# Kernel tuning notes

Measured on AMD Instinct MI355X. Metric: run time of the kernel, lower is better.

Reference implementation:

```python
import jax, jax.numpy as jnp
import numpy as np
import math

N_HEADS = 12
HEAD_DIM = 64
D_MODEL = 768
BATCH = 2
SEQ = 2048
GRID = 46  # num_patches_per_side


def _rope_1d(x, pos, dim):
    # x: (B,S,H,dim), pos: (S,) int -> rotary embedding along last dim
    inv_freq = 1.0 / (10000.0 ** (jnp.arange(0, dim, 2, dtype=jnp.float32) / dim))  # (dim/2,)
    ang = pos.astype(jnp.float32)[:, None] * inv_freq  # (S, dim/2)
    cos = jnp.concatenate([jnp.cos(ang), jnp.cos(ang)], axis=-1)[None, :, None, :]
    sin = jnp.concatenate([jnp.sin(ang), jnp.sin(ang)], axis=-1)[None, :, None, :]
    x1, x2 = jnp.split(x, 2, axis=-1)
    rot = jnp.concatenate([-x2, x1], axis=-1)
    return x * cos.astype(x.dtype) + rot * sin.astype(x.dtype)


def _rope_2d(x, row_ids, col_ids):
    # 2D RoPE: first half of head_dim rotated by row position, second half by column position
    half = x.shape[-1] // 2
    xr = _rope_1d(x[..., :half], row_ids, half)
    xc = _rope_1d(x[..., half:], col_ids, half)
    return jnp.concatenate([xr, xc], axis=-1)


def setup_inputs() -> dict:
    key = jax.random.key(0)
    ks = jax.random.split(key, 7)
    scale = 1.0 / math.sqrt(D_MODEL)
    return {
        "x": jax.random.normal(ks[0], (BATCH, SEQ, D_MODEL), dtype=jnp.float32),
        "row_ids": jax.random.randint(ks[1], (SEQ,), 0, GRID),
        "col_ids": jax.random.randint(ks[2], (SEQ,), 0, GRID),
        "Wq": jax.random.normal(ks[3], (D_MODEL, D_MODEL), dtype=jnp.float32) * scale,
        "Wk": jax.random.normal(ks[4], (D_MODEL, D_MODEL), dtype=jnp.float32) * scale,
        "Wv": jax.random.normal(ks[5], (D_MODEL, D_MODEL), dtype=jnp.float32) * scale,
        "Wo": jax.random.normal(ks[6], (D_MODEL, D_MODEL), dtype=jnp.float32) * scale,
    }


def reference(x, row_ids, col_ids, Wq, Wk, Wv, Wo):
    B, S, _ = x.shape
    # projections (nn.Linear: y = x @ W.T)
    q = (x @ Wq.T).reshape(B, S, N_HEADS, HEAD_DIM)
    k = (x @ Wk.T).reshape(B, S, N_HEADS, HEAD_DIM)
    v = (x @ Wv.T).reshape(B, S, N_HEADS, HEAD_DIM)
    q = _rope_2d(q, row_ids, col_ids)
    k = _rope_2d(k, row_ids, col_ids)
    # (B,H,S,D)
    q = q.transpose(0, 2, 1, 3)
    k = k.transpose(0, 2, 1, 3)
    v = v.transpose(0, 2, 1, 3)
    scale = 1.0 / math.sqrt(HEAD_DIM)
    scores = jnp.einsum('bhqd,bhkd->bhqk', q, k) * scale  # (B,H,S,S)
    causal = jnp.triu(jnp.ones((S, S), dtype=bool), k=1)
    scores = jnp.where(causal, -jnp.inf, scores)
    attn = jax.nn.softmax(scores, axis=-1)
    out = jnp.einsum('bhqk,bhkd->bhqd', attn, v)
    out = out.transpose(0, 2, 1, 3).reshape(B, S, D_MODEL)
    return out @ Wo.T
```

## Files before the change

### kernel.cpp

```cpp
#include <hip/hip_runtime.h>
#include <stdint.h>
#include <stddef.h>

#define DEV __device__ __forceinline__

typedef unsigned short u16;
typedef __attribute__((ext_vector_type(8))) __bf16 bf16x8;
typedef __attribute__((ext_vector_type(4))) float f32x4;
typedef __attribute__((ext_vector_type(8))) unsigned short u16x8;
typedef __attribute__((ext_vector_type(4))) unsigned short u16x4;

DEV u16 f2bf(float f) {
  uint32_t u = __builtin_bit_cast(uint32_t, f);
  u += 0x7fffu + ((u >> 16) & 1u);
  return (u16)(u >> 16);
}
DEV float bf2f(u16 h) {
  uint32_t u = ((uint32_t)h) << 16;
  return __builtin_bit_cast(float, u);
}
DEV f32x4 mfma16(bf16x8 a, bf16x8 b, f32x4 c) {
  return __builtin_amdgcn_mfma_f32_16x16x32_bf16(a, b, c, 0, 0, 0);
}
DEV void ld_lds16(const void* g, void* l) {
  __builtin_amdgcn_global_load_lds((const __attribute__((address_space(1))) void*)g,
                                   (__attribute__((address_space(3))) void*)l, 16, 0, 0);
}

#define Q_SCALE 0.18033688011112042f

__global__ __launch_bounds__(256) void k_cvt_all(const float* __restrict__ x,
                                                 const float* __restrict__ wq,
                                                 const float* __restrict__ wk,
                                                 const float* __restrict__ wv,
                                                 const float* __restrict__ wo,
                                                 u16* __restrict__ dx,
                                                 u16* __restrict__ dqkv,
                                                 u16* __restrict__ dwo) {
  const int bid = blockIdx.x;
  const float* src;
  u16* dst;
  int off;
  if (bid < 3072) {
    src = x; dst = dx; off = bid;
  } else {
    const int t = bid - 3072;
    const int w = t / 576;
    off = t - w * 576;
    src = (w == 0) ? wq : (w == 1) ? wk : (w == 2) ? wv : wo;
    dst = (w < 3) ? (dqkv + (size_t)w * 589824) : dwo;
  }
  const int i = (off * 256 + threadIdx.x) * 4;
  const float4 f = *(const float4*)(src + i);
  u16x4 o;
  o.x = f2bf(f.x); o.y = f2bf(f.y); o.z = f2bf(f.z); o.w = f2bf(f.w);
  *(u16x4*)(dst + i) = o;
}

__global__ __launch_bounds__(256) void k_gemm_qkv(const u16* __restrict__ A,
                                                  const u16* __restrict__ B,
                                                  const int* __restrict__ row_ids,
                                                  const int* __restrict__ col_ids,
                                                  u16* __restrict__ Qh,
                                                  u16* __restrict__ Kh,
                                                  u16* __restrict__ Vt) {
  const int K = 768;
  __shared__ __align__(16) u16 sA[128 * 64];
  __shared__ __align__(16) u16 sB[128 * 64];
  __shared__ int sIds[256];
  const int tid = threadIdx.x;
  const int lane = tid & 63;
  const int wid = tid >> 6;
  const int wm = wid & 1, wn = wid >> 1;
  const int col16 = lane & 15, quad = lane >> 4;
  const int rowBase = blockIdx.y * 128;
  const int colBase = blockIdx.x * 128;
  const int seg_r = lane >> 3;
  const int seg_c = lane & 7;

  f32x4 zero; zero[0] = zero[1] = zero[2] = zero[3] = 0.0f;
  f32x4 acc[4][4];
#pragma unroll
  for (int i = 0; i < 4; ++i)
#pragma unroll
    for (int j = 0; j < 4; ++j) acc[i][j] = zero;

  for (int k0 = 0; k0 < K; k0 += 64) {
#pragma unroll
    for (int c = 0; c < 4; ++c) {
      const int seg = wid * 4 + c;
      ld_lds16(A + (size_t)(rowBase + seg * 8 + seg_r) * K + k0 + seg_c * 8, sA + seg * 512);
      ld_lds16(B + (size_t)(colBase + seg * 8 + seg_r) * K + k0 + seg_c * 8, sB + seg * 512);
    }
    __syncthreads();
#pragma unroll
    for (int kk = 0; kk < 2; ++kk) {
      bf16x8 af[4], bfr[4];
#pragma unroll
      for (int t = 0; t < 4; ++t) {
        af[t]  = *(const bf16x8*)(sA + (wm * 64 + t * 16 + col16) * 64 + kk * 32 + quad * 8);
        bfr[t] = *(const bf16x8*)(sB + (wn * 64 + t * 16 + col16) * 64 + kk * 32 + quad * 8);
      }
#pragma unroll
      for (int tm = 0; tm < 4; ++tm)
#pragma unroll
        for (int tn = 0; tn < 4; ++tn)
          acc[tm][tn] = mfma16(af[tm], bfr[tn], acc[tm][tn]);
    }
    __syncthreads();
  }

  const int bx = blockIdx.x;
  const int type = bx / 6;
  const int h = (bx % 6) * 2 + wn;
  const int bb = rowBase >> 11;
  const int s0 = rowBase & 2047;
  const size_t bh = (size_t)bb * 12 + h;

  if (type < 2) {
    if (tid < 128) {
      sIds[tid] = row_ids[s0 + tid];
      sIds[128 + tid] = col_ids[s0 + tid];
    }
    __syncthreads();
    u16* dst = (type == 0) ? Qh : Kh;
    const float scl = (type == 0) ? Q_SCALE : 1.0f;
    const float invf = exp2f(-(float)col16 * 0.8304820237218406f);
#pragma unroll
    for (int tm = 0; tm < 4; ++tm)
#pragma unroll
      for (int r = 0; r < 4; ++r) {
        const int lrow = wm * 64 + tm * 16 + quad * 4 + r;
        const float aR = (float)sIds[lrow] * invf;
        const float aC = (float)sIds[128 + lrow] * invf;
        const float cR = __cosf(aR), sR = __sinf(aR);
        const float cC = __cosf(aC), sC = __sinf(aC);
        const float x1 = acc[tm][0][r], x2 = acc[tm][1][r];
        const float x3 = acc[tm][2][r], x4 = acc[tm][3][r];
        u16* p = dst + (bh * 2048 + s0 + lrow) * 64;
        p[col16]      = f2bf((x1 * cR - x2 * sR) * scl);
        p[col16 + 16] = f2bf((x2 * cR + x1 * sR) * scl);
        p[col16 + 32] = f2bf((x3 * cC - x4 * sC) * scl);
        p[col16 + 48] = f2bf((x4 * cC + x3 * sC) * scl);
      }
  } else {
#pragma unroll
    for (int tm = 0; tm < 4; ++tm)
#pragma unroll
      for (int tn = 0; tn < 4; ++tn) {
        const int d = tn * 16 + col16;
        const int srow = s0 + wm * 64 + tm * 16 + quad * 4;
        u16x4 o4;
#pragma unroll
        for (int r = 0; r < 4; ++r) o4[r] = f2bf(acc[tm][tn][r]);
        *(u16x4*)(Vt + (bh * 64 + d) * 2048 + srow) = o4;
      }
  }
}

__global__ __launch_bounds__(256, 3) void k_gemm_o(const u16* __restrict__ A,
                                                   const u16* __restrict__ B,
                                                   float* __restrict__ C,
                                                   int N, int K) {
  __shared__ __align__(16) u16 sA[64 * 72];
  __shared__ __align__(16) u16 sB[64 * 72];
  const int tid = threadIdx.x;
  const int lane = tid & 63;
  const int wid = tid >> 6;
  const int col16 = lane & 15, quad = lane >> 4;
  const int wm = wid & 1, wn = wid >> 1;
  const int rowBase = blockIdx.y * 64;
  const int colBase = blockIdx.x * 64;
  const int sr = tid >> 3;
  const int sc8 = (tid & 7) * 8;

  f32x4 zero; zero[0] = zero[1] = zero[2] = zero[3] = 0.0f;
  f32x4 acc[2][2];
  acc[0][0] = zero; acc[0][1] = zero; acc[1][0] = zero; acc[1][1] = zero;

  u16x8 ar[2], br[2];
  auto gload = [&](int k0) {
    ar[0] = *(const u16x8*)(A + (size_t)(rowBase + sr) * K + k0 + sc8);
    ar[1] = *(const u16x8*)(A + (size_t)(rowBase + 32 + sr) * K + k0 + sc8);
    br[0] = *(const u16x8*)(B + (size_t)(colBase + sr) * K + k0 + sc8);
    br[1] = *(const u16x8*)(B + (size_t)(colBase + 32 + sr) * K + k0 + sc8);
  };

  gload(0);
  for (int k0 = 0; k0 < K; k0 += 64) {
    __syncthreads();
    *(u16x8*)&sA[sr * 72 + sc8] = ar[0];
    *(u16x8*)&sA[(32 + sr) * 72 + sc8] = ar[1];
    *(u16x8*)&sB[sr * 72 + sc8] = br[0];
    *(u16x8*)&sB[(32 + sr) * 72 + sc8] = br[1];
    if (k0 + 64 < K) gload(k0 + 64);
    __syncthreads();
#pragma unroll
    for (int kk = 0; kk < 2; ++kk) {
      bf16x8 af[2], bfr[2];
#pragma unroll
      for (int t = 0; t < 2; ++t) {
        af[t]  = *(const bf16x8*)&sA[(wm * 32 + t * 16 + col16) * 72 + kk * 32 + quad * 8];
        bfr[t] = *(const bf16x8*)&sB[(wn * 32 + t * 16 + col16) * 72 + kk * 32 + quad * 8];
      }
#pragma unroll
      for (int tm = 0; tm < 2; ++tm)
#pragma unroll
        for (int tn = 0; tn < 2; ++tn)
          acc[tm][tn] = mfma16(af[tm], bfr[tn], acc[tm][tn]);
    }
  }

#pragma unroll
  for (int tm = 0; tm < 2; ++tm)
#pragma unroll
    for (int tn = 0; tn < 2; ++tn)
#pragma unroll
      for (int r = 0; r < 4; ++r) {
        const int row = rowBase + wm * 32 + tm * 16 + quad * 4 + r;
        const int col = colBase + wn * 32 + tn * 16 + col16;
        C[(size_t)row * N + col] = acc[tm][tn][r];
      }
}

__global__ __launch_bounds__(256, 3) void k_attn(const u16* __restrict__ Qh,
                                                 const u16* __restrict__ Kh,
                                                 const u16* __restrict__ Vt,
                                                 u16* __restrict__ O,
                                                 u16* __restrict__ Opart,
                                                 float* __restrict__ ml) {
  __shared__ __align__(16) u16 sK[2][64 * 72];
  __shared__ __align__(16) u16 sV[2][64 * 72];
  __shared__ __align__(16) u16 sP[4][16 * 72];
  const int tid = threadIdx.x;
  const int lane = tid & 63;
  const int wid = tid >> 6;
  const int col16 = lane & 15;
  const int quad = lane >> 4;
  const int bx = blockIdx.x;
  const int bh = bx / 80;
  const int u = bx - bh * 80;
  int qt, c;
  if (u < 8)       { qt = u; c = 0; }
  else if (u < 24) { const int t = u - 8;  qt = 8 + (t >> 1); c = t & 1; }
  else if (u < 48) { const int t = u - 24; const int q3 = t / 3; qt = 16 + q3; c = t - q3 * 3; }
  else             { const int t = u - 48; qt = 24 + (t >> 2); c = t & 3; }
  const int nc = (qt >> 3) + 1;
  const int tile0 = c * 8;
  const int tileE = min(tile0 + 8, qt + 1);
  const int ntiles = tileE - tile0;
  const int b = bh / 12, h = bh % 12;
  const int qw = qt * 64 + wid * 16;

  const u16* Qb = Qh + (size_t)bh * (2048 * 64);
  const u16* Kb = Kh + (size_t)bh * (2048 * 64);
  const u16* Vb = Vt + (size_t)bh * (64 * 2048);

  const bf16x8 bQ0 = *(const bf16x8*)(Qb + (size_t)(qw + col16) * 64 + quad * 8);
  const bf16x8 bQ1 = *(const bf16x8*)(Qb + (size_t)(qw + col16) * 64 + 32 + quad * 8);

  f32x4 zero; zero[0] = zero[1] = zero[2] = zero[3] = 0.0f;
  f32x4 o[4];
#pragma unroll
  for (int i = 0; i < 4; ++i) o[i] = zero;
  float m_r = -1e30f, l_r = 0.0f;

  u16* sPw = &sP[wid][0];

  const int sr = tid >> 3;
  const int sc8 = (tid & 7) * 8;
  u16x8 kr[2], vr[2];
  auto gload = [&](int kt) {
#pragma unroll
    for (int i = 0; i < 2; ++i) {
      kr[i] = *(const u16x8*)(Kb + (size_t)(kt + sr + i * 32) * 64 + sc8);
      vr[i] = *(const u16x8*)(Vb + (size_t)(sr + i * 32) * 2048 + kt + sc8);
    }
  };
  auto lwrite = [&](int buf) {
#pragma unroll
    for (int i = 0; i < 2; ++i) {
      *(u16x8*)&sK[buf][(sr + i * 32) * 72 + sc8] = kr[i];
      *(u16x8*)&sV[buf][(sr + i * 32) * 72 + sc8] = vr[i];
    }
  };

  gload(tile0 * 64);
  lwrite(0);
  if (ntiles > 1) gload((tile0 + 1) * 64);
  __syncthreads();

  for (int ki = 0; ki < ntiles; ++ki) {
    const int buf = ki & 1;
    const int kt = (tile0 + ki) * 64;
    if (ki + 1 < ntiles) {
      lwrite(buf ^ 1);
      if (ki + 2 < ntiles) gload((tile0 + ki + 2) * 64);
    }
    bf16x8 ka0[4], ka1[4];
#pragma unroll
    for (int tn = 0; tn < 4; ++tn) {
      const int base = (tn * 16 + col16) * 72 + quad * 8;
      ka0[tn] = *(const bf16x8*)&sK[buf][base];
      ka1[tn] = *(const bf16x8*)&sK[buf][base + 32];
    }
    f32x4 sc[4];
#pragma unroll
    for (int tn = 0; tn < 4; ++tn)
      sc[tn] = mfma16(ka1[tn], bQ1, mfma16(ka0[tn], bQ0, zero));
    bf16x8 va0[4], va1[4];
#pragma unroll
    for (int tn = 0; tn < 4; ++tn) {
      const int base = (tn * 16 + col16) * 72 + quad * 8;
      va0[tn] = *(const bf16x8*)&sV[buf][base];
      va1[tn] = *(const bf16x8*)&sV[buf][base + 32];
    }
    if (kt + 63 > qw) {
#pragma unroll
      for (int tn = 0; tn < 4; ++tn)
#pragma unroll
        for (int rr = 0; rr < 4; ++rr)
          if (kt + tn * 16 + quad * 4 + rr > qw + col16) sc[tn][rr] = -1e30f;
    }
    float vm = sc[0][0];
#pragma unroll
    for (int tn = 0; tn < 4; ++tn)
#pragma unroll
      for (int rr = 0; rr < 4; ++rr) vm = fmaxf(vm, sc[tn][rr]);
    vm = fmaxf(vm, __shfl_xor(vm, 16, 64));
    vm = fmaxf(vm, __shfl_xor(vm, 32, 64));
    const float mn = fmaxf(m_r, vm);
    const float alpha = exp2f(m_r - mn);
    m_r = mn;
    float rs = 0.0f;
#pragma unroll
    for (int tn = 0; tn < 4; ++tn)
#pragma unroll
      for (int h2 = 0; h2 < 2; ++h2) {
        const float p0 = exp2f(sc[tn][2 * h2] - mn);
        const float p1 = exp2f(sc[tn][2 * h2 + 1] - mn);
        const uint32_t u0 = __builtin_bit_cast(uint32_t, p0) & 0xffff0000u;
        const uint32_t u1 = __builtin_bit_cast(uint32_t, p1) & 0xffff0000u;
        rs += __builtin_bit_cast(float, u0) + __builtin_bit_cast(float, u1);
        ((uint32_t*)sPw)[col16 * 36 + tn * 8 + quad * 2 + h2] = u1 | (u0 >> 16);
      }
    rs += __shfl_xor(rs, 16, 64);
    rs += __shfl_xor(rs, 32, 64);
    l_r = l_r * alpha + rs;
#pragma unroll
    for (int t = 0; t < 4; ++t)
#pragma unroll
      for (int rr = 0; rr < 4; ++rr) o[t][rr] *= alpha;
    asm volatile("s_waitcnt lgkmcnt(0)" ::: "memory");
    const bf16x8 bP0 = *(const bf16x8*)(sPw + col16 * 72 + quad * 8);
    const bf16x8 bP1 = *(const bf16x8*)(sPw + col16 * 72 + 32 + quad * 8);
#pragma unroll
    for (int tn = 0; tn < 4; ++tn)
      o[tn] = mfma16(va1[tn], bP1, mfma16(va0[tn], bP0, o[tn]));
    __syncthreads();
  }

  if (nc == 1) {
    const float invl = 1.0f / l_r;
    const size_t row = (size_t)b * 2048 + qw + col16;
#pragma unroll
    for (int tn = 0; tn < 4; ++tn)
#pragma unroll
      for (int h2 = 0; h2 < 2; ++h2) {
        const float v0 = o[tn][2 * h2] * invl;
        const float v1 = o[tn][2 * h2 + 1] * invl;
        const uint32_t w = (uint32_t)f2bf(v0) | ((uint32_t)f2bf(v1) << 16);
        const int col = h * 64 + tn * 16 + quad * 4 + 2 * h2;
        *(uint32_t*)(O + row * 768 + col) = w;
      }
  } else {
    u16* op = Opart + (size_t)bx * 4096 + (wid * 16 + col16) * 64;
#pragma unroll
    for (int tn = 0; tn < 4; ++tn)
#pragma unroll
      for (int h2 = 0; h2 < 2; ++h2) {
        const uint32_t w = (uint32_t)f2bf(o[tn][2 * h2]) | ((uint32_t)f2bf(o[tn][2 * h2 + 1]) << 16);
        *(uint32_t*)(op + tn * 16 + quad * 4 + 2 * h2) = w;
      }
    if (quad == 0) {
      float* mlp = ml + (size_t)bx * 128;
      mlp[wid * 16 + col16] = m_r;
      mlp[64 + wid * 16 + col16] = l_r;
    }
  }
}

__global__ __launch_bounds__(256) void k_combine(const u16* __restrict__ Opart,
                                                 const float* __restrict__ ml,
                                                 u16* __restrict__ O) {
  const int bx = blockIdx.x;
  const int bh = bx / 24;
  const int qt = 8 + (bx - bh * 24);
  const int b = bh / 12, h = bh % 12;
  const int nc = (qt >> 3) + 1;
  const int prefix = (qt < 16) ? (8 + 2 * (qt - 8))
                   : (qt < 24) ? (24 + 3 * (qt - 16))
                               : (48 + 4 * (qt - 24));
  const int slot0 = bh * 80 + prefix;
  const int tid = threadIdx.x;
  const int r = tid >> 2;
  const int d0 = (tid & 3) * 16;

  float m_i[4], w_i[4];
  float M = -1e30f;
  for (int i = 0; i < nc; ++i) {
    m_i[i] = ml[(size_t)(slot0 + i) * 128 + r];
    M = fmaxf(M, m_i[i]);
  }
  float l = 0.0f;
  for (int i = 0; i < nc; ++i) {
    w_i[i] = exp2f(m_i[i] - M);
    l += w_i[i] * ml[(size_t)(slot0 + i) * 128 + 64 + r];
  }
  const float invl = 1.0f / l;

  float a[16];
#pragma unroll
  for (int j = 0; j < 16; ++j) a[j] = 0.0f;
  for (int i = 0; i < nc; ++i) {
    const u16* op = Opart + (size_t)(slot0 + i) * 4096 + r * 64 + d0;
    const u16x8 v0 = *(const u16x8*)op;
    const u16x8 v1 = *(const u16x8*)(op + 8);
#pragma unroll
    for (int j = 0; j < 8; ++j) {
      a[j] += w_i[i] * bf2f(v0[j]);
      a[8 + j] += w_i[i] * bf2f(v1[j]);
    }
  }
  u16x8 o0, o1;
#pragma unroll
  for (int j = 0; j < 8; ++j) {
    o0[j] = f2bf(a[j] * invl);
    o1[j] = f2bf(a[8 + j] * invl);
  }
  u16* dst = O + (size_t)(b * 2048 + qt * 64 + r) * 768 + h * 64 + d0;
  *(u16x8*)dst = o0;
  *(u16x8*)(dst + 8) = o1;
}

extern "C" void kernel_launch(void* const* d_in, const int* in_sizes, int n_in,
                              void* d_out, int out_size, void* d_ws, size_t ws_size,
                              hipStream_t stream) {
  const float* x       = (const float*)d_in[0];
  const int*   row_ids = (const int*)d_in[1];
  const int*   col_ids = (const int*)d_in[2];
  const float* Wq      = (const float*)d_in[3];
  const float* Wk      = (const float*)d_in[4];
  const float* Wv      = (const float*)d_in[5];
  const float* Wo      = (const float*)d_in[6];
  float* out = (float*)d_out;

  uint8_t* w8 = (uint8_t*)d_ws;
  u16* x_bf = (u16*)(w8 + 0);
  u16* wqkv = (u16*)(w8 + 6291456);
  u16* wo   = (u16*)(w8 + 9830400);
  u16* qh   = (u16*)(w8 + 29884416);
  u16* kh   = (u16*)(w8 + 36175872);
  u16* vt   = (u16*)(w8 + 42467328);
  u16* obuf = (u16*)(w8 + 48758784);
  u16*   opart = (u16*)(w8 + 11010048);
  float* mlbuf = (float*)(w8 + 11010048 + 15728640);

  k_cvt_all<<<5376, 256, 0, stream>>>(x, Wq, Wk, Wv, Wo, x_bf, wqkv, wo);
  k_gemm_qkv<<<dim3(18, 32), 256, 0, stream>>>(x_bf, wqkv, row_ids, col_ids, qh, kh, vt);
  k_attn<<<1920, 256, 0, stream>>>(qh, kh, vt, obuf, opart, mlbuf);
  k_combine<<<576, 256, 0, stream>>>(opart, mlbuf, obuf);
  k_gemm_o<<<dim3(12, 64), 256, 0, stream>>>(obuf, wo, out, 768, 768);
}
```

Before: 184.0 us.

## Process two query tiles per attention block to reuse K/V loads

Each attention block now handles 128 query rows (two 64-row groups per wave) instead of 64, so every K/V tile staged in LDS feeds twice as many MFMAs and the block count is halved. Block ordering is remapped to interleave heads and put the longest work first. The online-softmax rescale is skipped when the running max does not grow. The combine kernel and partial-buffer layout are updated to match, at the cost of more registers per thread and fewer blocks to fill the GPU.

```diff
diff --git a/kernel.cpp b/kernel.cpp
--- a/kernel.cpp
+++ b/kernel.cpp
@@ -238,32 +238,42 @@
   const int col16 = lane & 15;
   const int quad = lane >> 4;
   const int bx = blockIdx.x;
-  const int bh = bx / 80;
-  const int u = bx - bh * 80;
-  int qt, c;
-  if (u < 8)       { qt = u; c = 0; }
-  else if (u < 24) { const int t = u - 8;  qt = 8 + (t >> 1); c = t & 1; }
-  else if (u < 48) { const int t = u - 24; const int q3 = t / 3; qt = 16 + q3; c = t - q3 * 3; }
-  else             { const int t = u - 48; qt = 24 + (t >> 2); c = t & 3; }
-  const int nc = (qt >> 3) + 1;
+  const int b3 = bx & 7;
+  const int r_ = bx >> 3;
+  const int g_ = r_ / 40;
+  const int u = 39 - (r_ - g_ * 40);
+  const int bh = b3 + 8 * g_;
+  int qt2, c;
+  if (u < 4)       { qt2 = u; c = 0; }
+  else if (u < 12) { const int t = u - 4;  qt2 = 4 + (t >> 1); c = t & 1; }
+  else if (u < 24) { const int t = u - 12; const int q3 = t / 3; qt2 = 8 + q3; c = t - q3 * 3; }
+  else             { const int t = u - 24; qt2 = 12 + (t >> 2); c = t & 3; }
+  const int nc = (qt2 >> 2) + 1;
+  const int totTiles = 2 * qt2 + 2;
   const int tile0 = c * 8;
-  const int tileE = min(tile0 + 8, qt + 1);
-  const int ntiles = tileE - tile0;
+  const int ntiles = min(8, totTiles - tile0);
   const int b = bh / 12, h = bh % 12;
-  const int qw = qt * 64 + wid * 16;
+  const int qs0 = qt2 * 128 + wid * 16;
 
   const u16* Qb = Qh + (size_t)bh * (2048 * 64);
   const u16* Kb = Kh + (size_t)bh * (2048 * 64);
   const u16* Vb = Vt + (size_t)bh * (64 * 2048);
 
-  const bf16x8 bQ0 = *(const bf16x8*)(Qb + (size_t)(qw + col16) * 64 + quad * 8);
-  const bf16x8 bQ1 = *(const bf16x8*)(Qb + (size_t)(qw + col16) * 64 + 32 + quad * 8);
+  bf16x8 bQ[2][2];
+#pragma unroll
+  for (int g = 0; g < 2; ++g) {
+    const u16* qp = Qb + (size_t)(qs0 + g * 64 + col16) * 64 + quad * 8;
+    bQ[g][0] = *(const bf16x8*)qp;
+    bQ[g][1] = *(const bf16x8*)(qp + 32);
+  }
 
   f32x4 zero; zero[0] = zero[1] = zero[2] = zero[3] = 0.0f;
-  f32x4 o[4];
-#pragma unroll
-  for (int i = 0; i < 4; ++i) o[i] = zero;
-  float m_r = -1e30f, l_r = 0.0f;
+  f32x4 o[2][4];
+#pragma unroll
+  for (int g = 0; g < 2; ++g)
+#pragma unroll
+    for (int i = 0; i < 4; ++i) o[g][i] = zero;
+  float m_r[2] = {-1e30f, -1e30f}, l_r[2] = {0.0f, 0.0f};
 
   u16* sPw = &sP[wid][0];
 
@@ -304,10 +314,12 @@
       ka0[tn] = *(const bf16x8*)&sK[buf][base];
       ka1[tn] = *(const bf16x8*)&sK[buf][base + 32];
     }
-    f32x4 sc[4];
-#pragma unroll
-    for (int tn = 0; tn < 4; ++tn)
-      sc[tn] = mfma16(ka1[tn], bQ1, mfma16(ka0[tn], bQ0, zero));
+    f32x4 sc[2][4];
+#pragma unroll
+    for (int tn = 0; tn < 4; ++tn) {
+      sc[0][tn] = mfma16(ka1[tn], bQ[0][1], mfma16(ka0[tn], bQ[0][0], zero));
+      sc[1][tn] = mfma16(ka1[tn], bQ[1][1], mfma16(ka0[tn], bQ[1][0], zero));
+    }
     bf16x8 va0[4], va1[4];
 #pragma unroll
     for (int tn = 0; tn < 4; ++tn) {
@@ -315,77 +327,93 @@
       va0[tn] = *(const bf16x8*)&sV[buf][base];
       va1[tn] = *(const bf16x8*)&sV[buf][base + 32];
     }
-    if (kt + 63 > qw) {
+#pragma unroll
+    for (int g = 0; g < 2; ++g) {
+      const int qw = qs0 + g * 64;
+      if (kt + 63 > qw) {
+#pragma unroll
+        for (int tn = 0; tn < 4; ++tn)
+#pragma unroll
+          for (int rr = 0; rr < 4; ++rr)
+            if (kt + tn * 16 + quad * 4 + rr > qw + col16) sc[g][tn][rr] = -1e30f;
+      }
+      float vm = sc[g][0][0];
 #pragma unroll
       for (int tn = 0; tn < 4; ++tn)
 #pragma unroll
-        for (int rr = 0; rr < 4; ++rr)
-          if (kt + tn * 16 + quad * 4 + rr > qw + col16) sc[tn][rr] = -1e30f;
-    }
-    float vm = sc[0][0];
-#pragma unroll
-    for (int tn = 0; tn < 4; ++tn)
-#pragma unroll
-      for (int rr = 0; rr < 4; ++rr) vm = fmaxf(vm, sc[tn][rr]);
-    vm = fmaxf(vm, __shfl_xor(vm, 16, 64));
-    vm = fmaxf(vm, __shfl_xor(vm, 32, 64));
-    const float mn = fmaxf(m_r, vm);
-    const float alpha = exp2f(m_r - mn);
-    m_r = mn;
-    float rs = 0.0f;
-#pragma unroll
-    for (int tn = 0; tn < 4; ++tn)
-#pragma unroll
-      for (int h2 = 0; h2 < 2; ++h2) {
-        const float p0 = exp2f(sc[tn][2 * h2] - mn);
-        const float p1 = exp2f(sc[tn][2 * h2 + 1] - mn);
-        const uint32_t u0 = __builtin_bit_cast(uint32_t, p0) & 0xffff0000u;
-        const uint32_t u1 = __builtin_bit_cast(uint32_t, p1) & 0xffff0000u;
-        rs += __builtin_bit_cast(float, u0) + __builtin_bit_cast(float, u1);
-        ((uint32_t*)sPw)[col16 * 36 + tn * 8 + quad * 2 + h2] = u1 | (u0 >> 16);
-      }
-    rs += __shfl_xor(rs, 16, 64);
-    rs += __shfl_xor(rs, 32, 64);
-    l_r = l_r * alpha + rs;
-#pragma unroll
-    for (int t = 0; t < 4; ++t)
-#pragma unroll
-      for (int rr = 0; rr < 4; ++rr) o[t][rr] *= alpha;
-    asm volatile("s_waitcnt lgkmcnt(0)" ::: "memory");
-    const bf16x8 bP0 = *(const bf16x8*)(sPw + col16 * 72 + quad * 8);
-    const bf16x8 bP1 = *(const bf16x8*)(sPw + col16 * 72 + 32 + quad * 8);
-#pragma unroll
-    for (int tn = 0; tn < 4; ++tn)
-      o[tn] = mfma16(va1[tn], bP1, mfma16(va0[tn], bP0, o[tn]));
+        for (int rr = 0; rr < 4; ++rr) vm = fmaxf(vm, sc[g][tn][rr]);
+      vm = fmaxf(vm, __shfl_xor(vm, 16, 64));
+      vm = fmaxf(vm, __shfl_xor(vm, 32, 64));
+      if (__any(vm > m_r[g])) {
+        const float mn = fmaxf(m_r[g], vm);
+        const float alpha = exp2f(m_r[g] - mn);
+        m_r[g] = mn;
+        l_r[g] *= alpha;
+#pragma unroll
+        for (int t = 0; t < 4; ++t)
+#pragma unroll
+          for (int rr = 0; rr < 4; ++rr) o[g][t][rr] *= alpha;
+      }
+      const float mn = m_r[g];
+      float rs = 0.0f;
+#pragma unroll
+      for (int tn = 0; tn < 4; ++tn)
+#pragma unroll
+        for (int h2 = 0; h2 < 2; ++h2) {
+          const float p0 = exp2f(sc[g][tn][2 * h2] - mn);
+          const float p1 = exp2f(sc[g][tn][2 * h2 + 1] - mn);
+          const uint32_t u0 = __builtin_bit_cast(uint32_t, p0) & 0xffff0000u;
+          const uint32_t u1 = __builtin_bit_cast(uint32_t, p1) & 0xffff0000u;
+          rs += __builtin_bit_cast(float, u0) + __builtin_bit_cast(float, u1);
+          ((uint32_t*)sPw)[col16 * 36 + tn * 8 + quad * 2 + h2] = u1 | (u0 >> 16);
+        }
+      rs += __shfl_xor(rs, 16, 64);
+      rs += __shfl_xor(rs, 32, 64);
+      l_r[g] += rs;
+      asm volatile("s_waitcnt lgkmcnt(0)" ::: "memory");
+      const bf16x8 bP0 = *(const bf16x8*)(sPw + col16 * 72 + quad * 8);
+      const bf16x8 bP1 = *(const bf16x8*)(sPw + col16 * 72 + 32 + quad * 8);
+#pragma unroll
+      for (int tn = 0; tn < 4; ++tn)
+        o[g][tn] = mfma16(va1[tn], bP1, mfma16(va0[tn], bP0, o[g][tn]));
+    }
     __syncthreads();
   }
 
   if (nc == 1) {
-    const float invl = 1.0f / l_r;
-    const size_t row = (size_t)b * 2048 + qw + col16;
-#pragma unroll
-    for (int tn = 0; tn < 4; ++tn)
-#pragma unroll
-      for (int h2 = 0; h2 < 2; ++h2) {
-        const float v0 = o[tn][2 * h2] * invl;
-        const float v1 = o[tn][2 * h2 + 1] * invl;
-        const uint32_t w = (uint32_t)f2bf(v0) | ((uint32_t)f2bf(v1) << 16);
-        const int col = h * 64 + tn * 16 + quad * 4 + 2 * h2;
-        *(uint32_t*)(O + row * 768 + col) = w;
-      }
+#pragma unroll
+    for (int g = 0; g < 2; ++g) {
+      const float invl = 1.0f / l_r[g];
+      const size_t row = (size_t)b * 2048 + qs0 + g * 64 + col16;
+#pragma unroll
+      for (int tn = 0; tn < 4; ++tn)
+#pragma unroll
+        for (int h2 = 0; h2 < 2; ++h2) {
+          const float v0 = o[g][tn][2 * h2] * invl;
+          const float v1 = o[g][tn][2 * h2 + 1] * invl;
+          const uint32_t w = (uint32_t)f2bf(v0) | ((uint32_t)f2bf(v1) << 16);
+          const int col = h * 64 + tn * 16 + quad * 4 + 2 * h2;
+          *(uint32_t*)(O + row * 768 + col) = w;
+        }
+    }
   } else {
-    u16* op = Opart + (size_t)bx * 4096 + (wid * 16 + col16) * 64;
-#pragma unroll
-    for (int tn = 0; tn < 4; ++tn)
-#pragma unroll
-      for (int h2 = 0; h2 < 2; ++h2) {
-        const uint32_t w = (uint32_t)f2bf(o[tn][2 * h2]) | ((uint32_t)f2bf(o[tn][2 * h2 + 1]) << 16);
-        *(uint32_t*)(op + tn * 16 + quad * 4 + 2 * h2) = w;
-      }
-    if (quad == 0) {
-      float* mlp = ml + (size_t)bx * 128;
-      mlp[wid * 16 + col16] = m_r;
-      mlp[64 + wid * 16 + col16] = l_r;
+#pragma unroll
+    for (int g = 0; g < 2; ++g) {
+      const int prow = g * 64 + wid * 16 + col16;
+      u16* op = Opart + (size_t)bx * 8192 + prow * 64;
+#pragma unroll
+      for (int tn = 0; tn < 4; ++tn)
+#pragma unroll
+        for (int h2 = 0; h2 < 2; ++h2) {
+          const uint32_t w = (uint32_t)f2bf(o[g][tn][2 * h2]) |
+                             ((uint32_t)f2bf(o[g][tn][2 * h2 + 1]) << 16);
+          *(uint32_t*)(op + tn * 16 + quad * 4 + 2 * h2) = w;
+        }
+      if (quad == 0) {
+        float* mlp = ml + (size_t)bx * 256;
+        mlp[prow] = m_r[g];
+        mlp[128 + prow] = l_r[g];
+      }
     }
   }
 }
@@ -394,53 +422,55 @@
                                                  const float* __restrict__ ml,
                                                  u16* __restrict__ O) {
   const int bx = blockIdx.x;
-  const int bh = bx / 24;
-  const int qt = 8 + (bx - bh * 24);
+  const int bh = bx / 12;
+  const int qt2 = 4 + (bx - bh * 12);
   const int b = bh / 12, h = bh % 12;
-  const int nc = (qt >> 3) + 1;
-  const int prefix = (qt < 16) ? (8 + 2 * (qt - 8))
-                   : (qt < 24) ? (24 + 3 * (qt - 16))
-                               : (48 + 4 * (qt - 24));
-  const int slot0 = bh * 80 + prefix;
+  const int nc = (qt2 >> 2) + 1;
+  const int uBase = (qt2 < 8) ? (4 + 2 * (qt2 - 4))
+                  : (qt2 < 12) ? (12 + 3 * (qt2 - 8))
+                               : (24 + 4 * (qt2 - 12));
+  const int hb3 = bh & 7, hg = bh >> 3;
   const int tid = threadIdx.x;
-  const int r = tid >> 2;
-  const int d0 = (tid & 3) * 16;
+  const int r = tid >> 1;
+  const int d0 = (tid & 1) * 32;
+
+  int slots[4];
+  for (int i = 0; i < nc; ++i)
+    slots[i] = ((hg * 40 + 39 - (uBase + i)) << 3) | hb3;
 
   float m_i[4], w_i[4];
   float M = -1e30f;
   for (int i = 0; i < nc; ++i) {
-    m_i[i] = ml[(size_t)(slot0 + i) * 128 + r];
+    m_i[i] = ml[(size_t)slots[i] * 256 + r];
     M = fmaxf(M, m_i[i]);
   }
   float l = 0.0f;
   for (int i = 0; i < nc; ++i) {
     w_i[i] = exp2f(m_i[i] - M);
-    l += w_i[i] * ml[(size_t)(slot0 + i) * 128 + 64 + r];
+    l += w_i[i] * ml[(size_t)slots[i] * 256 + 128 + r];
   }
   const float invl = 1.0f / l;
 
-  float a[16];
-#pragma unroll
-  for (int j = 0; j < 16; ++j) a[j] = 0.0f;
+  float a[32];
+#pragma unroll
+  for (int j = 0; j < 32; ++j) a[j] = 0.0f;
   for (int i = 0; i < nc; ++i) {
-    const u16* op = Opart + (size_t)(slot0 + i) * 4096 + r * 64 + d0;
-    const u16x8 v0 = *(const u16x8*)op;
-    const u16x8 v1 = *(const u16x8*)(op + 8);
-#pragma unroll
-    for (int j = 0; j < 8; ++j) {
-      a[j] += w_i[i] * bf2f(v0[j]);
-      a[8 + j] += w_i[i] * bf2f(v1[j]);
-    }
-  }
-  u16x8 o0, o1;
-#pragma unroll
-  for (int j = 0; j < 8; ++j) {
-    o0[j] = f2bf(a[j] * invl);
-    o1[j] = f2bf(a[8 + j] * invl);
-  }
-  u16* dst = O + (size_t)(b * 2048 + qt * 64 + r) * 768 + h * 64 + d0;
-  *(u16x8*)dst = o0;
-  *(u16x8*)(dst + 8) = o1;
+    const u16* op = Opart + (size_t)slots[i] * 8192 + r * 64 + d0;
+#pragma unroll
+    for (int v = 0; v < 4; ++v) {
+      const u16x8 vv = *(const u16x8*)(op + v * 8);
+#pragma unroll
+      for (int j = 0; j < 8; ++j) a[v * 8 + j] += w_i[i] * bf2f(vv[j]);
+    }
+  }
+  u16* dst = O + (size_t)(b * 2048 + qt2 * 128 + r) * 768 + h * 64 + d0;
+#pragma unroll
+  for (int v = 0; v < 4; ++v) {
+    u16x8 ov;
+#pragma unroll
+    for (int j = 0; j < 8; ++j) ov[j] = f2bf(a[v * 8 + j] * invl);
+    *(u16x8*)(dst + v * 8) = ov;
+  }
 }
 
 extern "C" void kernel_launch(void* const* d_in, const int* in_sizes, int n_in,
@@ -468,7 +498,7 @@
 
   k_cvt_all<<<5376, 256, 0, stream>>>(x, Wq, Wk, Wv, Wo, x_bf, wqkv, wo);
   k_gemm_qkv<<<dim3(18, 32), 256, 0, stream>>>(x_bf, wqkv, row_ids, col_ids, qh, kh, vt);
-  k_attn<<<1920, 256, 0, stream>>>(qh, kh, vt, obuf, opart, mlbuf);
-  k_combine<<<576, 256, 0, stream>>>(opart, mlbuf, obuf);
+  k_attn<<<960, 256, 0, stream>>>(qh, kh, vt, obuf, opart, mlbuf);
+  k_combine<<<288, 256, 0, stream>>>(opart, mlbuf, obuf);
   k_gemm_o<<<dim3(12, 64), 256, 0, stream>>>(obuf, wo, out, 768, 768);
 }
```

Result: no change. 187.4 us (+1.9%).

## Shrink QKV GEMM tile to 64 rows, pack RoPE stores, widen conversion loads

Applied to the files above, without the earlier changes.

The QKV projection GEMM now uses 64x128 tiles, so twice as many blocks launch and each wave owns one 32-column RoPE half. That lets each lane compute a single sin/cos pair and write packed 32-bit pairs. The output dims within each half are permuted identically for Q and K, so the dot products are unchanged. The fp32-to-bf16 conversion kernel handles 8 elements per thread with 16-byte stores, and the attention P conversion now rounds to nearest instead of truncating. The smaller tile reloads B from memory more often, in exchange for better occupancy and lighter epilogue work.

```diff
diff --git a/kernel.cpp b/kernel.cpp
--- a/kernel.cpp
+++ b/kernel.cpp
@@ -41,70 +41,74 @@
   const float* src;
   u16* dst;
   int off;
-  if (bid < 3072) {
+  if (bid < 1536) {
     src = x; dst = dx; off = bid;
   } else {
-    const int t = bid - 3072;
-    const int w = t / 576;
-    off = t - w * 576;
+    const int t = bid - 1536;
+    const int w = t / 288;
+    off = t - w * 288;
     src = (w == 0) ? wq : (w == 1) ? wk : (w == 2) ? wv : wo;
     dst = (w < 3) ? (dqkv + (size_t)w * 589824) : dwo;
   }
-  const int i = (off * 256 + threadIdx.x) * 4;
-  const float4 f = *(const float4*)(src + i);
-  u16x4 o;
-  o.x = f2bf(f.x); o.y = f2bf(f.y); o.z = f2bf(f.z); o.w = f2bf(f.w);
-  *(u16x4*)(dst + i) = o;
-}
-
-__global__ __launch_bounds__(256) void k_gemm_qkv(const u16* __restrict__ A,
-                                                  const u16* __restrict__ B,
-                                                  const int* __restrict__ row_ids,
-                                                  const int* __restrict__ col_ids,
-                                                  u16* __restrict__ Qh,
-                                                  u16* __restrict__ Kh,
-                                                  u16* __restrict__ Vt) {
+  const int i = (off * 256 + threadIdx.x) * 8;
+  const float4 f0 = *(const float4*)(src + i);
+  const float4 f1 = *(const float4*)(src + i + 4);
+  u16x8 o;
+  o[0] = f2bf(f0.x); o[1] = f2bf(f0.y); o[2] = f2bf(f0.z); o[3] = f2bf(f0.w);
+  o[4] = f2bf(f1.x); o[5] = f2bf(f1.y); o[6] = f2bf(f1.z); o[7] = f2bf(f1.w);
+  *(u16x8*)(dst + i) = o;
+}
+
+__global__ __launch_bounds__(256, 4) void k_gemm_qkv(const u16* __restrict__ A,
+                                                     const u16* __restrict__ B,
+                                                     const int* __restrict__ row_ids,
+                                                     const int* __restrict__ col_ids,
+                                                     u16* __restrict__ Qh,
+                                                     u16* __restrict__ Kh,
+                                                     u16* __restrict__ Vt) {
   const int K = 768;
-  __shared__ __align__(16) u16 sA[128 * 64];
+  __shared__ __align__(16) u16 sA[64 * 64];
   __shared__ __align__(16) u16 sB[128 * 64];
-  __shared__ int sIds[256];
+  __shared__ int sIds[128];
   const int tid = threadIdx.x;
   const int lane = tid & 63;
   const int wid = tid >> 6;
-  const int wm = wid & 1, wn = wid >> 1;
   const int col16 = lane & 15, quad = lane >> 4;
-  const int rowBase = blockIdx.y * 128;
+  const int rowBase = blockIdx.y * 64;
   const int colBase = blockIdx.x * 128;
   const int seg_r = lane >> 3;
   const int seg_c = lane & 7;
 
   f32x4 zero; zero[0] = zero[1] = zero[2] = zero[3] = 0.0f;
-  f32x4 acc[4][4];
-#pragma unroll
-  for (int i = 0; i < 4; ++i)
-#pragma unroll
-    for (int j = 0; j < 4; ++j) acc[i][j] = zero;
+  f32x4 acc[4][2];
+#pragma unroll
+  for (int i = 0; i < 4; ++i) { acc[i][0] = zero; acc[i][1] = zero; }
 
   for (int k0 = 0; k0 < K; k0 += 64) {
+#pragma unroll
+    for (int c = 0; c < 2; ++c) {
+      const int seg = wid * 2 + c;
+      ld_lds16(A + (size_t)(rowBase + seg * 8 + seg_r) * K + k0 + seg_c * 8, sA + seg * 512);
+    }
 #pragma unroll
     for (int c = 0; c < 4; ++c) {
       const int seg = wid * 4 + c;
-      ld_lds16(A + (size_t)(rowBase + seg * 8 + seg_r) * K + k0 + seg_c * 8, sA + seg * 512);
       ld_lds16(B + (size_t)(colBase + seg * 8 + seg_r) * K + k0 + seg_c * 8, sB + seg * 512);
     }
     __syncthreads();
 #pragma unroll
     for (int kk = 0; kk < 2; ++kk) {
-      bf16x8 af[4], bfr[4];
-#pragma unroll
-      for (int t = 0; t < 4; ++t) {
-        af[t]  = *(const bf16x8*)(sA + (wm * 64 + t * 16 + col16) * 64 + kk * 32 + quad * 8);
-        bfr[t] = *(const bf16x8*)(sB + (wn * 64 + t * 16 + col16) * 64 + kk * 32 + quad * 8);
-      }
+      bf16x8 af[4], bfr[2];
+#pragma unroll
+      for (int t = 0; t < 4; ++t)
+        af[t] = *(const bf16x8*)(sA + (t * 16 + col16) * 64 + kk * 32 + quad * 8);
+#pragma unroll
+      for (int t = 0; t < 2; ++t)
+        bfr[t] = *(const bf16x8*)(sB + (wid * 32 + t * 16 + col16) * 64 + kk * 32 + quad * 8);
 #pragma unroll
       for (int tm = 0; tm < 4; ++tm)
 #pragma unroll
-        for (int tn = 0; tn < 4; ++tn)
+        for (int tn = 0; tn < 2; ++tn)
           acc[tm][tn] = mfma16(af[tm], bfr[tn], acc[tm][tn]);
     }
     __syncthreads();
@@ -112,44 +116,41 @@
 
   const int bx = blockIdx.x;
   const int type = bx / 6;
-  const int h = (bx % 6) * 2 + wn;
+  const int h = (bx % 6) * 2 + (wid >> 1);
+  const int half = wid & 1;
   const int bb = rowBase >> 11;
   const int s0 = rowBase & 2047;
   const size_t bh = (size_t)bb * 12 + h;
 
   if (type < 2) {
-    if (tid < 128) {
-      sIds[tid] = row_ids[s0 + tid];
-      sIds[128 + tid] = col_ids[s0 + tid];
-    }
+    if (tid < 64) sIds[tid] = row_ids[s0 + tid];
+    else if (tid < 128) sIds[tid] = col_ids[s0 + tid - 64];
     __syncthreads();
     u16* dst = (type == 0) ? Qh : Kh;
     const float scl = (type == 0) ? Q_SCALE : 1.0f;
     const float invf = exp2f(-(float)col16 * 0.8304820237218406f);
+    const int idOff = half * 64;
 #pragma unroll
     for (int tm = 0; tm < 4; ++tm)
 #pragma unroll
       for (int r = 0; r < 4; ++r) {
-        const int lrow = wm * 64 + tm * 16 + quad * 4 + r;
-        const float aR = (float)sIds[lrow] * invf;
-        const float aC = (float)sIds[128 + lrow] * invf;
-        const float cR = __cosf(aR), sR = __sinf(aR);
-        const float cC = __cosf(aC), sC = __sinf(aC);
+        const int lrow = tm * 16 + quad * 4 + r;
+        const float ang = (float)sIds[idOff + lrow] * invf;
+        const float cs = __cosf(ang), sn = __sinf(ang);
         const float x1 = acc[tm][0][r], x2 = acc[tm][1][r];
-        const float x3 = acc[tm][2][r], x4 = acc[tm][3][r];
+        const float y1 = (x1 * cs - x2 * sn) * scl;
+        const float y2 = (x2 * cs + x1 * sn) * scl;
         u16* p = dst + (bh * 2048 + s0 + lrow) * 64;
-        p[col16]      = f2bf((x1 * cR - x2 * sR) * scl);
-        p[col16 + 16] = f2bf((x2 * cR + x1 * sR) * scl);
-        p[col16 + 32] = f2bf((x3 * cC - x4 * sC) * scl);
-        p[col16 + 48] = f2bf((x4 * cC + x3 * sC) * scl);
+        *(uint32_t*)(p + half * 32 + 2 * col16) =
+            (uint32_t)f2bf(y1) | ((uint32_t)f2bf(y2) << 16);
       }
   } else {
 #pragma unroll
     for (int tm = 0; tm < 4; ++tm)
 #pragma unroll
-      for (int tn = 0; tn < 4; ++tn) {
-        const int d = tn * 16 + col16;
-        const int srow = s0 + wm * 64 + tm * 16 + quad * 4;
+      for (int tn = 0; tn < 2; ++tn) {
+        const int d = half * 32 + tn * 16 + col16;
+        const int srow = s0 + tm * 16 + quad * 4;
         u16x4 o4;
 #pragma unroll
         for (int r = 0; r < 4; ++r) o4[r] = f2bf(acc[tm][tn][r]);
@@ -339,10 +340,9 @@
       for (int h2 = 0; h2 < 2; ++h2) {
         const float p0 = exp2f(sc[tn][2 * h2] - mn);
         const float p1 = exp2f(sc[tn][2 * h2 + 1] - mn);
-        const uint32_t u0 = __builtin_bit_cast(uint32_t, p0) & 0xffff0000u;
-        const uint32_t u1 = __builtin_bit_cast(uint32_t, p1) & 0xffff0000u;
-        rs += __builtin_bit_cast(float, u0) + __builtin_bit_cast(float, u1);
-        ((uint32_t*)sPw)[col16 * 36 + tn * 8 + quad * 2 + h2] = u1 | (u0 >> 16);
+        rs += p0 + p1;
+        const uint32_t w = (uint32_t)f2bf(p0) | ((uint32_t)f2bf(p1) << 16);
+        ((uint32_t*)sPw)[col16 * 36 + tn * 8 + quad * 2 + h2] = w;
       }
     rs += __shfl_xor(rs, 16, 64);
     rs += __shfl_xor(rs, 32, 64);
@@ -466,8 +466,8 @@
   u16*   opart = (u16*)(w8 + 11010048);
   float* mlbuf = (float*)(w8 + 11010048 + 15728640);
 
-  k_cvt_all<<<5376, 256, 0, stream>>>(x, Wq, Wk, Wv, Wo, x_bf, wqkv, wo);
-  k_gemm_qkv<<<dim3(18, 32), 256, 0, stream>>>(x_bf, wqkv, row_ids, col_ids, qh, kh, vt);
+  k_cvt_all<<<2688, 256, 0, stream>>>(x, Wq, Wk, Wv, Wo, x_bf, wqkv, wo);
+  k_gemm_qkv<<<dim3(18, 64), 256, 0, stream>>>(x_bf, wqkv, row_ids, col_ids, qh, kh, vt);
   k_attn<<<1920, 256, 0, stream>>>(qh, kh, vt, obuf, opart, mlbuf);
   k_combine<<<576, 256, 0, stream>>>(opart, mlbuf, obuf);
   k_gemm_o<<<dim3(12, 64), 256, 0, stream>>>(obuf, wo, out, 768, 768);
```

New measurement: 172.6 us. 6.2% less time.
